# Kernel tuning notes

Measured on AMD Instinct MI355X. Metric: run time of the kernel, lower is better.

## Reference

```python
import jax, jax.numpy as jnp
import numpy as np
from jax import lax

B, N, IN_DIM = 8, 196, 2048
C = 256          # conv_channels / subspace dim
G = 1            # relation_glimpse


def _dilated_conv(x, w, b, dil):
    # x: [B,N,N,Cin], w: [3,3,Cin,Cout], SAME padding, rhs dilation per source
    y = lax.conv_general_dilated(x, w, window_strides=(1, 1), padding='SAME',
                                 rhs_dilation=dil,
                                 dimension_numbers=('NHWC', 'HWIO', 'NHWC'))
    return y + b


def _rel_map(X):
    # X: [B,N,N,G] -> symmetric add, move glimpse to axis 1, softmax over N*N
    Xs = X + jnp.transpose(X, (0, 2, 1, 3))          # [B,N,N,G]
    m = jnp.transpose(Xs, (0, 3, 2, 1))              # [B,G,N,N]
    bsz, g, n, _ = m.shape
    m = jax.nn.softmax(m.reshape(bsz, g, n * n), axis=2)
    return m.reshape(bsz, g, n, n)


def setup_inputs() -> dict:
    key = jax.random.key(0)
    ks = jax.random.split(key, 8)
    s = lambda *sh: 1.0 / np.sqrt(sh[-2] if len(sh) > 1 else sh[0])
    return {
        'x': jax.random.normal(ks[0], (B, N, IN_DIM), jnp.float32),
        'w_prj': jax.random.normal(ks[1], (IN_DIM, C), jnp.float32) * 0.02,
        'b_prj': jnp.zeros((C,), jnp.float32),
        'w01': jax.random.normal(ks[2], (C, C // 2), jnp.float32) * 0.06,
        'b01': jnp.zeros((C // 2,), jnp.float32),
        'w02': jax.random.normal(ks[3], (C // 2, C // 4), jnp.float32) * 0.09,
        'b02': jnp.zeros((C // 4,), jnp.float32),
        'w03': jax.random.normal(ks[4], (C // 4, G), jnp.float32) * 0.125,
        'b03': jnp.zeros((G,), jnp.float32),
        'w1': jax.random.normal(ks[5], (3, 3, C, C // 2), jnp.float32) * 0.02,
        'b1': jnp.zeros((C // 2,), jnp.float32),
        'w2': jax.random.normal(ks[6], (3, 3, C // 2, C // 4), jnp.float32) * 0.03,
        'b2': jnp.zeros((C // 4,), jnp.float32),
        'w3': jax.random.normal(ks[7], (3, 3, C // 4, G), jnp.float32) * 0.04,
        'b3': jnp.zeros((G,), jnp.float32),
    }


def reference(x, w_prj, b_prj, w01, b01, w02, b02, w03, b03,
              w1, b1, w2, b2, w3, b3):
    # project to subspace: [B,N,C]
    sub = jnp.einsum('bnd,dc->bnc', x, w_prj) + b_prj
    # pairwise outer product: pair[b,i,j,c] = sub[b,i,c]*sub[b,j,c]
    pair = sub[:, :, None, :] * sub[:, None, :, :]          # [B,N,N,C]

    # branch 0: stacked 1x1 convs (pointwise) with relu; dropout = identity (eval)
    X0 = jax.nn.relu(jnp.einsum('bijc,cd->bijd', pair, w01) + b01)
    X0 = jax.nn.relu(jnp.einsum('bijc,cd->bijd', X0, w02) + b02)
    X0 = jax.nn.relu(jnp.einsum('bijc,cd->bijd', X0, w03) + b03)  # [B,N,N,G]
    rel_map0 = _rel_map(X0)                                  # [B,G,N,N]

    # branch 1: stacked 3x3 dilated convs, dilations (1,1),(1,2),(1,4)
    X1 = jax.nn.relu(_dilated_conv(pair, w1, b1, (1, 1)))
    X1 = jax.nn.relu(_dilated_conv(X1, w2, b2, (1, 2)))
    X1 = jax.nn.relu(_dilated_conv(X1, w3, b3, (1, 4)))      # [B,N,N,G]
    rel_map1 = _rel_map(X1)

    # aggregation over glimpses: rel_x = sum_g (map1[g]@x + map0[g]@x) / (2G)
    rel_x = (jnp.einsum('bgij,bjd->bid', rel_map1, x) +
             jnp.einsum('bgij,bjd->bid', rel_map0, x)) / (2.0 * G)
    return rel_x.reshape(x.shape[0], -1)                     # [B, N*in_dim]
```

## Files before the change

kernel.cpp:

```cpp
#include <hip/hip_runtime.h>
#include <cmath>

#define N_TOK 196
#define NPX   38416
#define CDIM  256

typedef _Float16 f16;
typedef __attribute__((ext_vector_type(8))) _Float16 half8;
typedef __attribute__((ext_vector_type(4))) float f32x4;

__global__ __launch_bounds__(256) void proj_mfma(
    const float* __restrict__ A,
    const float* __restrict__ B,
    float* __restrict__ P)
{
    __shared__ f16 As[128 * 40];
    __shared__ f16 Bs[128 * 40];
    int tid = threadIdx.x;
    int n0 = blockIdx.x * 128, m0 = blockIdx.y * 128;
    int kz = blockIdx.z;
    int wave = tid >> 6, lane = tid & 63;
    int quad = lane >> 4, l16 = lane & 15;

    f32x4 zero = {0.f, 0.f, 0.f, 0.f};
    f32x4 acc[2][8];
    #pragma unroll
    for (int mt = 0; mt < 2; ++mt)
        #pragma unroll
        for (int nt = 0; nt < 8; ++nt) acc[mt][nt] = zero;

    for (int k0 = kz * 256; k0 < kz * 256 + 256; k0 += 32) {
        __syncthreads();
        #pragma unroll
        for (int s = 0; s < 4; ++s) {
            int idx = tid + s * 256;
            int m = idx >> 3, kq = idx & 7;
            int gm = m0 + m;
            float4 v = make_float4(0.f, 0.f, 0.f, 0.f);
            if (gm < 1568) v = *(const float4*)(A + (size_t)gm * 2048 + k0 + kq * 4);
            f16* d = As + m * 40 + kq * 4;
            d[0] = (f16)v.x; d[1] = (f16)v.y; d[2] = (f16)v.z; d[3] = (f16)v.w;
        }
        #pragma unroll
        for (int s = 0; s < 4; ++s) {
            int idx = tid + s * 256;
            int nq = idx & 31, kk = idx >> 5;
            float4 v = *(const float4*)(B + (size_t)(k0 + kk) * 256 + n0 + nq * 4);
            Bs[(nq * 4 + 0) * 40 + kk] = (f16)v.x;
            Bs[(nq * 4 + 1) * 40 + kk] = (f16)v.y;
            Bs[(nq * 4 + 2) * 40 + kk] = (f16)v.z;
            Bs[(nq * 4 + 3) * 40 + kk] = (f16)v.w;
        }
        __syncthreads();
        half8 a[2];
        #pragma unroll
        for (int mt = 0; mt < 2; ++mt)
            a[mt] = *(const half8*)(As + (wave * 32 + mt * 16 + l16) * 40 + quad * 8);
        #pragma unroll
        for (int nt = 0; nt < 8; ++nt) {
            half8 bf = *(const half8*)(Bs + (nt * 16 + l16) * 40 + quad * 8);
            acc[0][nt] = __builtin_amdgcn_mfma_f32_16x16x32_f16(a[0], bf, acc[0][nt], 0, 0, 0);
            acc[1][nt] = __builtin_amdgcn_mfma_f32_16x16x32_f16(a[1], bf, acc[1][nt], 0, 0, 0);
        }
    }
    float* Pz = P + (size_t)kz * 401408;
    #pragma unroll
    for (int mt = 0; mt < 2; ++mt) {
        #pragma unroll
        for (int nt = 0; nt < 8; ++nt) {
            int gn = n0 + nt * 16 + l16;
            #pragma unroll
            for (int r = 0; r < 4; ++r) {
                int gm = m0 + wave * 32 + mt * 16 + quad * 4 + r;
                if (gm < 1568) Pz[(size_t)gm * 256 + gn] = acc[mt][nt][r];
            }
        }
    }
}

__global__ void reduce_subh(const float* __restrict__ P,
                            const float* __restrict__ bias,
                            f16* __restrict__ subh)
{
    int e = blockIdx.x * 256 + threadIdx.x;
    if (e >= 401408) return;
    float s = bias[e & 255];
    #pragma unroll
    for (int z = 0; z < 8; ++z) s += P[(size_t)z * 401408 + e];
    subh[e] = (f16)s;
}

__global__ void cvt_wt(const float* __restrict__ w, f16* __restrict__ wt,
                       int Kc, int D, int total)
{
    int e = blockIdx.x * 256 + threadIdx.x;
    if (e >= total) return;
    int td = Kc * D;
    int tap = e / td, r = e - tap * td;
    int c = r / D, d = r - c * D;
    wt[(size_t)(tap * D + d) * Kc + c] = (f16)w[e];
}

__global__ void cvt_wfrag(const float* __restrict__ w, f16* __restrict__ wf,
                          int Kc, int D, int taps)
{
    int tiles = D >> 4, kch = Kc >> 5;
    int total = taps * tiles * kch * 64;
    int e = blockIdx.x * 256 + threadIdx.x;
    if (e >= total) return;
    int lane = e & 63;
    int rest = e >> 6;
    int k = rest % kch; rest /= kch;
    int tile = rest % tiles;
    int tap = rest / tiles;
    int l16 = lane & 15, quad = lane >> 4;
    const float* src = w + ((size_t)tap * Kc + k * 32 + quad * 8) * D + tile * 16 + l16;
    f16* dst = wf + (size_t)e * 8;
    #pragma unroll
    for (int j = 0; j < 8; ++j) dst[j] = (f16)src[(size_t)j * D];
}

__global__ __launch_bounds__(256) void cvt_xT(const float* __restrict__ x,
                                              f16* __restrict__ xht)
{
    __shared__ float t[32][33];
    int b = blockIdx.z;
    int i0 = blockIdx.y * 32, n0 = blockIdx.x * 32;
    const float* xb = x + (size_t)b * 196 * 2048;
    for (int e = threadIdx.x; e < 1024; e += 256) {
        int r = e >> 5, c = e & 31;
        int gi = i0 + r;
        t[r][c] = (gi < 196) ? xb[(size_t)gi * 2048 + n0 + c] : 0.f;
    }
    __syncthreads();
    f16* xb2 = xht + (size_t)b * 2048 * 200;
    for (int e = threadIdx.x; e < 1024; e += 256) {
        int nl = e >> 5, il = e & 31;
        int gi = i0 + il, gn = n0 + nl;
        if (gi < 200) xb2[(size_t)gn * 200 + gi] = (f16)t[il][nl];
    }
}

__global__ __launch_bounds__(256, 2) void conv1_mfma(
    const f16* __restrict__ sub_h,
    const f16* __restrict__ w1f,
    const float* __restrict__ b1,
    f16* __restrict__ Y1h)
{
    __shared__ f16 sh[17408];
    f16* SJ = sh;
    f16* SI = sh + 8976;
    f16* OT = sh;

    int b = blockIdx.z;
    int i0 = blockIdx.y * 8, j0 = blockIdx.x * 32;
    int tid = threadIdx.x;
    const f16* subB = sub_h + (size_t)b * N_TOK * CDIM;

    uint4 zz = make_uint4(0, 0, 0, 0);
    for (int e = tid; e < 1088; e += 256) {
        int r = e >> 5, q = e & 31;
        int gj = j0 - 1 + r;
        uint4 v = zz;
        if (gj >= 0 && gj < N_TOK) v = *(const uint4*)(subB + gj * CDIM + q * 8);
        *(uint4*)(SJ + r * 264 + q * 8) = v;
    }
    for (int e = tid; e < 320; e += 256) {
        int r = e >> 5, q = e & 31;
        int gi = i0 - 1 + r;
        uint4 v = zz;
        if (gi >= 0 && gi < N_TOK) v = *(const uint4*)(subB + gi * CDIM + q * 8);
        *(uint4*)(SI + r * 264 + q * 8) = v;
    }
    __syncthreads();

    int wave = tid >> 6, lane = tid & 63;
    int quad = lane >> 4, l16 = lane & 15;
    int p  = wave >> 1;
    int dh = wave & 1;
    int d0 = dh * 64;

    float bias_r[4];
    #pragma unroll
    for (int n = 0; n < 4; ++n) bias_r[n] = b1[d0 + n * 16 + l16];

    const f16* wbase = w1f + (size_t)lane * 8 + (size_t)dh * 4 * 4096;

    int lb = blockIdx.x + 7 * (blockIdx.y + 25 * blockIdx.z);
    int rot = (lb * 3 + wave) & 7;

    f32x4 zero = {0.f, 0.f, 0.f, 0.f};
    f32x4 acc[8][4];
    #pragma unroll
    for (int m = 0; m < 8; ++m)
        #pragma unroll
        for (int n = 0; n < 4; ++n) acc[m][n] = zero;

    for (int kk = 0; kk < 8; ++kk) {
        int k = (kk + rot) & 7;
        int c0 = k * 32;
        half8 si[6];
        #pragma unroll
        for (int r = 0; r < 6; ++r)
            si[r] = *(const half8*)(SI + (p * 4 + r) * 264 + c0 + quad * 8);
        half8 sj[2][3];
        #pragma unroll
        for (int jf = 0; jf < 2; ++jf)
            #pragma unroll
            for (int dd = 0; dd < 3; ++dd)
                sj[jf][dd] = *(const half8*)(SJ + (jf * 16 + l16 + dd) * 264 + c0 + quad * 8);

        #pragma unroll
        for (int dj = 0; dj < 3; ++dj) {
            half8 bf[3][4];
            #pragma unroll
            for (int di = 0; di < 3; ++di)
                #pragma unroll
                for (int n = 0; n < 4; ++n)
                    bf[di][n] = *(const half8*)(wbase + (size_t)(di * 3 + dj) * 32768
                                                + n * 4096 + k * 512);
            #pragma unroll
            for (int r = 0; r < 6; ++r) {
                half8 a0 = si[r] * sj[0][dj];
                half8 a1 = si[r] * sj[1][dj];
                #pragma unroll
                for (int di = 0; di < 3; ++di) {
                    int i = r - di;
                    if (i < 0 || i > 3) continue;
                    #pragma unroll
                    for (int n = 0; n < 4; ++n) {
                        acc[i * 2 + 0][n] = __builtin_amdgcn_mfma_f32_16x16x32_f16(
                            a0, bf[di][n], acc[i * 2 + 0][n], 0, 0, 0);
                        acc[i * 2 + 1][n] = __builtin_amdgcn_mfma_f32_16x16x32_f16(
                            a1, bf[di][n], acc[i * 2 + 1][n], 0, 0, 0);
                    }
                }
            }
        }
    }

    __syncthreads();
    f16* Yb = Y1h + (size_t)b * NPX * 128;
    #pragma unroll
    for (int ph = 0; ph < 2; ++ph) {
        if (p == ph) {
            #pragma unroll
            for (int i = 0; i < 4; ++i)
                #pragma unroll
                for (int jf = 0; jf < 2; ++jf) {
                    int m = i * 2 + jf;
                    #pragma unroll
                    for (int n = 0; n < 4; ++n) {
                        int dl = d0 + n * 16 + l16;
                        #pragma unroll
                        for (int r = 0; r < 4; ++r) {
                            int pxl = i * 32 + jf * 16 + quad * 4 + r;
                            OT[pxl * 136 + dl] = (f16)fmaxf(acc[m][n][r] + bias_r[n], 0.f);
                        }
                    }
                }
        }
        __syncthreads();
        for (int e = tid; e < 2048; e += 256) {
            int pxl = e >> 4, q = e & 15;
            int gi = i0 + ph * 4 + (pxl >> 5), gj = j0 + (pxl & 31);
            if (gi < N_TOK && gj < N_TOK)
                *(uint4*)(Yb + ((size_t)gi * N_TOK + gj) * 128 + q * 8) =
                    *(const uint4*)(OT + pxl * 136 + q * 8);
        }
        __syncthreads();
    }
}

__global__ __launch_bounds__(256, 2) void conv2_mfma(
    const f16* __restrict__ Y1h, const f16* __restrict__ w2f,
    const float* __restrict__ b2, f16* __restrict__ Y2h)
{
    __shared__ f16 sh[29376];
    f16* Ys = sh;
    f16* OT = sh;

    int b = blockIdx.z;
    int i0 = blockIdx.y * 4, j0 = blockIdx.x * 32;
    int tid = threadIdx.x;
    const f16* Yb = Y1h + (size_t)b * NPX * 128;

    uint4 zz = make_uint4(0, 0, 0, 0);
    for (int e = tid; e < 3456; e += 256) {
        int ir = e / 576, rem = e - ir * 576;
        int jq = rem >> 4, q = rem & 15;
        int gi = i0 - 1 + ir, gj = j0 - 2 + jq;
        uint4 v = zz;
        if (gi >= 0 && gi < N_TOK && gj >= 0 && gj < N_TOK)
            v = *(const uint4*)(Yb + ((size_t)gi * N_TOK + gj) * 128 + q * 8);
        *(uint4*)(Ys + (ir * 36 + jq) * 136 + q * 8) = v;
    }
    __syncthreads();

    int wave = tid >> 6, lane = tid & 63;
    int quad = lane >> 4, l16 = lane & 15;
    int ii = wave;

    const f16* wbase = w2f + (size_t)lane * 8;

    f32x4 zero = {0.f, 0.f, 0.f, 0.f};
    f32x4 acc[2][4];
    #pragma unroll
    for (int jf = 0; jf < 2; ++jf)
        #pragma unroll
        for (int n = 0; n < 4; ++n) acc[jf][n] = zero;

    #pragma unroll
    for (int tap = 0; tap < 9; ++tap) {
        int di = tap / 3 - 1, dj2 = (tap % 3 - 1) * 2;
        #pragma unroll
        for (int k = 0; k < 4; ++k) {
            int c0 = k * 32;
            half8 a0 = *(const half8*)(Ys + ((ii + di + 1) * 36 + l16 + dj2 + 2) * 136
                                       + c0 + quad * 8);
            half8 a1 = *(const half8*)(Ys + ((ii + di + 1) * 36 + 16 + l16 + dj2 + 2) * 136
                                       + c0 + quad * 8);
            #pragma unroll
            for (int n = 0; n < 4; ++n) {
                half8 bf = *(const half8*)(wbase + (size_t)tap * 8192 + n * 2048 + k * 512);
                acc[0][n] = __builtin_amdgcn_mfma_f32_16x16x32_f16(a0, bf, acc[0][n], 0, 0, 0);
                acc[1][n] = __builtin_amdgcn_mfma_f32_16x16x32_f16(a1, bf, acc[1][n], 0, 0, 0);
            }
        }
    }
    __syncthreads();
    #pragma unroll
    for (int jf = 0; jf < 2; ++jf)
        #pragma unroll
        for (int n = 0; n < 4; ++n) {
            int d = n * 16 + l16;
            float bias = b2[d];
            #pragma unroll
            for (int r = 0; r < 4; ++r) {
                int px = ii * 32 + jf * 16 + quad * 4 + r;
                OT[px * 72 + d] = (f16)fmaxf(acc[jf][n][r] + bias, 0.f);
            }
        }
    __syncthreads();
    f16* Zb = Y2h + (size_t)b * NPX * 64;
    for (int e = tid; e < 1024; e += 256) {
        int px = e >> 3, q = e & 7;
        int i = i0 + (px >> 5), j = j0 + (px & 31);
        if (j < N_TOK)
            *(uint4*)(Zb + ((size_t)i * N_TOK + j) * 64 + q * 8) =
                *(const uint4*)(OT + px * 72 + q * 8);
    }
}

__global__ __launch_bounds__(256) void conv3_s(
    const f16* __restrict__ Y2h, const float* __restrict__ w3,
    const float* __restrict__ b3, float* __restrict__ X1)
{
    __shared__ f16 Ys[10 * 40 * 68];
    __shared__ float ws[576];
    int b = blockIdx.z;
    int i0 = blockIdx.y * 8, j0 = blockIdx.x * 32;
    int tid = threadIdx.x;
    const f16* Yb = Y2h + (size_t)b * NPX * 64;
    for (int e = tid; e < 576; e += 256) ws[e] = w3[e];
    uint4 zz = make_uint4(0, 0, 0, 0);
    for (int e = tid; e < 3200; e += 256) {
        int r = e / 320, rem = e - r * 320;
        int jq = rem >> 3, q = rem & 7;
        int gi = i0 - 1 + r, gj = j0 - 4 + jq;
        uint4 v = zz;
        if (gi >= 0 && gi < N_TOK && gj >= 0 && gj < N_TOK)
            v = *(const uint4*)(Yb + ((size_t)gi * N_TOK + gj) * 64 + q * 8);
        *(uint4*)(Ys + (r * 40 + jq) * 68 + q * 8) = v;
    }
    __syncthreads();
    int q = tid & 7, jl = (tid >> 3) & 31;
    float* Xb = X1 + (size_t)b * NPX;
    float bb = b3[0];
    #pragma unroll
    for (int il = 0; il < 8; ++il) {
        float s = 0.f;
        #pragma unroll
        for (int tap = 0; tap < 9; ++tap) {
            int di = tap / 3 - 1, dj4 = (tap % 3 - 1) * 4;
            half8 h = *(const half8*)(Ys + ((il + 1 + di) * 40 + jl + 4 + dj4) * 68 + q * 8);
            #pragma unroll
            for (int e = 0; e < 8; ++e) s += (float)h[e] * ws[tap * 64 + q * 8 + e];
        }
        s += __shfl_xor(s, 1);
        s += __shfl_xor(s, 2);
        s += __shfl_xor(s, 4);
        if (q == 0) {
            int gi = i0 + il, gj = j0 + jl;
            if (gi < N_TOK && gj < N_TOK)
                Xb[gi * N_TOK + gj] = fmaxf(s + bb, 0.f);
        }
    }
}

__global__ __launch_bounds__(256, 2) void branch0_mfma(
    const f16* __restrict__ sub_h,
    const f16* __restrict__ w01t,
    const float* __restrict__ b01,
    const f16* __restrict__ w02t,
    const float* __restrict__ b02,
    const float* __restrict__ w03, const float* __restrict__ b03,
    float* __restrict__ X0)
{
    __shared__ f16 sh[32000];
    __shared__ float W3s[64];
    f16* SJ = sh;
    f16* SI = sh + 8448;
    f16* BW = sh + 9472;
    f16* H1 = sh + 14592;
    f16* H2 = sh;

    int b = blockIdx.z;
    int i0 = blockIdx.y * 4, j0 = blockIdx.x * 32;
    int tid = threadIdx.x;
    const f16* subB = sub_h + (size_t)b * N_TOK * CDIM;

    uint4 zz = make_uint4(0, 0, 0, 0);
    for (int e = tid; e < 1024; e += 256) {
        int r = e >> 5, q = e & 31;
        int gj = j0 + r;
        uint4 v = zz;
        if (gj < N_TOK) v = *(const uint4*)(subB + gj * CDIM + q * 8);
        *(uint4*)(SJ + r * 264 + q * 8) = v;
    }
    if (tid < 128) {
        int r = tid >> 5, q = tid & 31;
        int gi = i0 + r;
        uint4 v = zz;
        if (gi < N_TOK) v = *(const uint4*)(subB + gi * CDIM + q * 8);
        *(uint4*)(SI + r * 256 + q * 8) = v;
    }
    if (tid < 64) W3s[tid] = w03[tid];

    int wave = tid >> 6, lane = tid & 63;
    int quad = lane >> 4, l16 = lane & 15;
    int ii = wave;

    f32x4 zero = {0.f, 0.f, 0.f, 0.f};
    f32x4 acc[2][8];
    #pragma unroll
    for (int t = 0; t < 2; ++t)
        #pragma unroll
        for (int n = 0; n < 8; ++n) acc[t][n] = zero;

    for (int c0 = 0; c0 < 256; c0 += 32) {
        __syncthreads();
        for (int e = tid; e < 512; e += 256) {
            int d = e >> 2, q = e & 3;
            *(uint4*)(BW + d * 40 + q * 8) =
                *(const uint4*)(w01t + (size_t)d * 256 + c0 + q * 8);
        }
        __syncthreads();
        half8 sib = *(const half8*)(SI + ii * 256 + c0 + quad * 8);
        half8 a0 = sib * *(const half8*)(SJ + l16 * 264 + c0 + quad * 8);
        half8 a1 = sib * *(const half8*)(SJ + (l16 + 16) * 264 + c0 + quad * 8);
        #pragma unroll
        for (int n = 0; n < 8; ++n) {
            half8 bf = *(const half8*)(BW + (n * 16 + l16) * 40 + quad * 8);
            acc[0][n] = __builtin_amdgcn_mfma_f32_16x16x32_f16(a0, bf, acc[0][n], 0, 0, 0);
            acc[1][n] = __builtin_amdgcn_mfma_f32_16x16x32_f16(a1, bf, acc[1][n], 0, 0, 0);
        }
    }
    #pragma unroll
    for (int t = 0; t < 2; ++t)
        #pragma unroll
        for (int n = 0; n < 8; ++n) {
            int d = n * 16 + l16;
            float bias = b01[d];
            #pragma unroll
            for (int r = 0; r < 4; ++r) {
                int px = ii * 32 + t * 16 + quad * 4 + r;
                H1[px * 136 + d] = (f16)fmaxf(acc[t][n][r] + bias, 0.f);
            }
        }

    f32x4 acc2[2][4];
    #pragma unroll
    for (int t = 0; t < 2; ++t)
        #pragma unroll
        for (int n = 0; n < 4; ++n) acc2[t][n] = zero;

    for (int c0 = 0; c0 < 128; c0 += 32) {
        __syncthreads();
        {
            int d = tid >> 2, q = tid & 3;
            if (d < 64)
                *(uint4*)(BW + d * 40 + q * 8) =
                    *(const uint4*)(w02t + (size_t)d * 128 + c0 + q * 8);
        }
        __syncthreads();
        half8 a0 = *(const half8*)(H1 + (ii * 32 + l16) * 136 + c0 + quad * 8);
        half8 a1 = *(const half8*)(H1 + (ii * 32 + 16 + l16) * 136 + c0 + quad * 8);
        #pragma unroll
        for (int n = 0; n < 4; ++n) {
            half8 bf = *(const half8*)(BW + (n * 16 + l16) * 40 + quad * 8);
            acc2[0][n] = __builtin_amdgcn_mfma_f32_16x16x32_f16(a0, bf, acc2[0][n], 0, 0, 0);
            acc2[1][n] = __builtin_amdgcn_mfma_f32_16x16x32_f16(a1, bf, acc2[1][n], 0, 0, 0);
        }
    }
    #pragma unroll
    for (int t = 0; t < 2; ++t)
        #pragma unroll
        for (int n = 0; n < 4; ++n) {
            int e = n * 16 + l16;
            float bias = b02[e];
            #pragma unroll
            for (int r = 0; r < 4; ++r) {
                int px = ii * 32 + t * 16 + quad * 4 + r;
                H2[px * 72 + e] = (f16)fmaxf(acc2[t][n][r] + bias, 0.f);
            }
        }
    __syncthreads();
    if (tid < 128) {
        int px = tid;
        float s = b03[0];
        const f16* h = H2 + px * 72;
        #pragma unroll 8
        for (int c = 0; c < 64; ++c) s += (float)h[c] * W3s[c];
        int i = i0 + (px >> 5), j = j0 + (px & 31);
        if (j < N_TOK)
            X0[(size_t)b * NPX + i * N_TOK + j] = fmaxf(s, 0.f);
    }
}

__global__ __launch_bounds__(1024) void symsoftmax(float* __restrict__ X0,
                                                   float* __restrict__ X1)
{
    __shared__ float red[32];
    __shared__ float red2[32];
    float* X = (blockIdx.y ? X1 : X0) + (long long)blockIdx.x * NPX;
    int tid = threadIdx.x;
    float v[38];
    float mx = -3.0e38f;
    #pragma unroll
    for (int p = 0; p < 38; ++p) {
        int e = tid + p * 1024;
        if (e < NPX) {
            int i = e / 196, j = e - i * 196;
            float t = X[e] + X[j * 196 + i];
            v[p] = t;
            mx = fmaxf(mx, t);
        } else v[p] = -3.0e38f;
    }
    #pragma unroll
    for (int off = 32; off > 0; off >>= 1) mx = fmaxf(mx, __shfl_xor(mx, off));
    if ((tid & 63) == 0) red[tid >> 6] = mx;
    __syncthreads();
    if (tid < 64) {
        float m = (tid < 16) ? red[tid] : -3.0e38f;
        #pragma unroll
        for (int off = 8; off > 0; off >>= 1) m = fmaxf(m, __shfl_xor(m, off));
        if (tid == 0) red[0] = m;
    }
    __syncthreads();
    mx = red[0];
    float s = 0.f;
    #pragma unroll
    for (int p = 0; p < 38; ++p) {
        int e = tid + p * 1024;
        float ex = (e < NPX) ? expf(v[p] - mx) : 0.f;
        v[p] = ex;
        s += ex;
    }
    #pragma unroll
    for (int off = 32; off > 0; off >>= 1) s += __shfl_xor(s, off);
    if ((tid & 63) == 0) red2[tid >> 6] = s;
    __syncthreads();
    if (tid < 64) {
        float m = (tid < 16) ? red2[tid] : 0.f;
        #pragma unroll
        for (int off = 8; off > 0; off >>= 1) m += __shfl_xor(m, off);
        if (tid == 0) red2[0] = m;
    }
    __syncthreads();
    float scale = 0.5f / red2[0];
    #pragma unroll
    for (int p = 0; p < 38; ++p) {
        int e = tid + p * 1024;
        if (e < NPX) X[e] = v[p] * scale;
    }
}

__global__ void combine_ph(const float* __restrict__ X0,
                           const float* __restrict__ X1,
                           f16* __restrict__ Ph)
{
    int e = blockIdx.x * 256 + threadIdx.x;
    if (e >= 8 * 196 * 200) return;
    int j = e % 200;
    int row = e / 200;
    f16 v = (f16)0.f;
    if (j < 196) {
        int src = row * 196 + j;
        v = (f16)((X0[src] + X1[src]) * 512.0f);
    }
    Ph[e] = v;
}

__global__ __launch_bounds__(256, 2) void gemm_out(
    const f16* __restrict__ Ph, const f16* __restrict__ xht,
    float* __restrict__ out)
{
    __shared__ f16 As[64 * 72];
    __shared__ f16 Bs[128 * 72];
    int b = blockIdx.z;
    int n0 = blockIdx.x * 128, m0 = blockIdx.y * 64;
    int tid = threadIdx.x;
    const f16* Pb = Ph + (size_t)b * 196 * 200;
    const f16* xb = xht + (size_t)b * 2048 * 200;

    int wave = tid >> 6, lane = tid & 63;
    int quad = lane >> 4, l16 = lane & 15;

    f32x4 zero = {0.f, 0.f, 0.f, 0.f};
    f32x4 acc[8];
    #pragma unroll
    for (int n = 0; n < 8; ++n) acc[n] = zero;

    uint4 zz = make_uint4(0, 0, 0, 0);
    for (int k0 = 0; k0 < 256; k0 += 64) {
        __syncthreads();
        for (int e = tid; e < 512; e += 256) {
            int r = e >> 3, q = e & 7;
            int gm = m0 + r, k = k0 + q * 8;
            uint4 v = zz;
            if (gm < 196 && k < 200) v = *(const uint4*)(Pb + (size_t)gm * 200 + k);
            *(uint4*)(As + r * 72 + q * 8) = v;
        }
        for (int e = tid; e < 1024; e += 256) {
            int r = e >> 3, q = e & 7;
            int k = k0 + q * 8;
            uint4 v = zz;
            if (k < 200) v = *(const uint4*)(xb + (size_t)(n0 + r) * 200 + k);
            *(uint4*)(Bs + r * 72 + q * 8) = v;
        }
        __syncthreads();
        #pragma unroll
        for (int ks = 0; ks < 2; ++ks) {
            half8 a = *(const half8*)(As + (wave * 16 + l16) * 72 + ks * 32 + quad * 8);
            #pragma unroll
            for (int n = 0; n < 8; ++n) {
                half8 bf = *(const half8*)(Bs + (n * 16 + l16) * 72 + ks * 32 + quad * 8);
                acc[n] = __builtin_amdgcn_mfma_f32_16x16x32_f16(a, bf, acc[n], 0, 0, 0);
            }
        }
    }
    int m_base = m0 + wave * 16 + quad * 4;
    float* ob = out + (size_t)b * 196 * 2048;
    #pragma unroll
    for (int n = 0; n < 8; ++n) {
        int gn = n0 + n * 16 + l16;
        #pragma unroll
        for (int r = 0; r < 4; ++r) {
            int gm = m_base + r;
            if (gm < 196) ob[(size_t)gm * 2048 + gn] = acc[n][r] * (1.0f / 512.0f);
        }
    }
}

extern "C" void kernel_launch(void* const* d_in, const int* in_sizes, int n_in,
                              void* d_out, int out_size, void* d_ws, size_t ws_size,
                              hipStream_t stream)
{
    (void)in_sizes; (void)n_in; (void)out_size; (void)ws_size;
    const float* x     = (const float*)d_in[0];
    const float* w_prj = (const float*)d_in[1];
    const float* b_prj = (const float*)d_in[2];
    const float* w01   = (const float*)d_in[3];
    const float* b01   = (const float*)d_in[4];
    const float* w02   = (const float*)d_in[5];
    const float* b02   = (const float*)d_in[6];
    const float* w03   = (const float*)d_in[7];
    const float* b03   = (const float*)d_in[8];
    const float* w1    = (const float*)d_in[9];
    const float* b1    = (const float*)d_in[10];
    const float* w2    = (const float*)d_in[11];
    const float* b2    = (const float*)d_in[12];
    const float* w3    = (const float*)d_in[13];
    const float* b3    = (const float*)d_in[14];

    char* W = (char*)d_ws;
    float* part = (float*)(W + 0);
    float* X0   = (float*)(W + 12845056);
    float* X1   = (float*)(W + 14074368);
    f16*   subh = (f16*)(W + 15303680);
    f16*   w1f  = (f16*)(W + 16106496);
    f16*   w2f  = (f16*)(W + 16696320);
    f16*   w01t = (f16*)(W + 16843776);
    f16*   w02t = (f16*)(W + 16909312);
    f16*   Ph   = (f16*)(W + 16925696);
    f16*   xht  = (f16*)(W + 17552896);
    f16*   Y1h  = (f16*)(W + 24106496);
    f16*   Y2h  = (f16*)(W + 102782464);

    proj_mfma<<<dim3(2, 13, 8), 256, 0, stream>>>(x, w_prj, part);
    reduce_subh<<<dim3(1568), 256, 0, stream>>>(part, b_prj, subh);

    cvt_wfrag<<<dim3(144), 256, 0, stream>>>(w1, w1f, 256, 128, 9);
    cvt_wfrag<<<dim3(36),  256, 0, stream>>>(w2, w2f, 128, 64, 9);
    cvt_wt<<<dim3(128),  256, 0, stream>>>(w01, w01t, 256, 128, 32768);
    cvt_wt<<<dim3(32),   256, 0, stream>>>(w02, w02t, 128, 64, 8192);
    cvt_xT<<<dim3(64, 7, 8), 256, 0, stream>>>(x, xht);

    branch0_mfma<<<dim3(7, 49, 8), 256, 0, stream>>>(
        subh, w01t, b01, w02t, b02, w03, b03, X0);

    conv1_mfma<<<dim3(7, 25, 8), 256, 0, stream>>>(subh, w1f, b1, Y1h);
    conv2_mfma<<<dim3(7, 49, 8), 256, 0, stream>>>(Y1h, w2f, b2, Y2h);
    conv3_s<<<dim3(7, 25, 8), 256, 0, stream>>>(Y2h, w3, b3, X1);

    symsoftmax<<<dim3(8, 2), 1024, 0, stream>>>(X0, X1);

    combine_ph<<<dim3(1225), 256, 0, stream>>>(X0, X1, Ph);

    gemm_out<<<dim3(16, 4, 8), 256, 0, stream>>>(Ph, xht, (float*)d_out);
}
```

Before: 513.9 us.

## Split conv1 work across 16 waves per block with smaller per-wave tiles

Conv1 now launches 1024 threads per block instead of 256. Each of the 16 waves computes 2 output rows by 32 output channels instead of 4 rows by 64 channels, which cuts accumulator registers from 32 to 8 fragments per wave. The goal is higher occupancy and more latency hiding, without changing the tile or the shared-memory footprint. The cost is that each wave reloads the si/sj operands and the weight fragments relative to the work it does, so redundant LDS and global weight loads go up.

```diff
diff --git a/kernel.cpp b/kernel.cpp
--- a/kernel.cpp
+++ b/kernel.cpp
@@ -141,7 +141,7 @@
     }
 }
 
-__global__ __launch_bounds__(256, 2) void conv1_mfma(
+__global__ __launch_bounds__(1024, 4) void conv1_mfma(
     const f16* __restrict__ sub_h,
     const f16* __restrict__ w1f,
     const float* __restrict__ b1,
@@ -158,14 +158,14 @@
     const f16* subB = sub_h + (size_t)b * N_TOK * CDIM;
 
     uint4 zz = make_uint4(0, 0, 0, 0);
-    for (int e = tid; e < 1088; e += 256) {
+    for (int e = tid; e < 1088; e += 1024) {
         int r = e >> 5, q = e & 31;
         int gj = j0 - 1 + r;
         uint4 v = zz;
         if (gj >= 0 && gj < N_TOK) v = *(const uint4*)(subB + gj * CDIM + q * 8);
         *(uint4*)(SJ + r * 264 + q * 8) = v;
     }
-    for (int e = tid; e < 320; e += 256) {
+    for (int e = tid; e < 320; e += 1024) {
         int r = e >> 5, q = e & 31;
         int gi = i0 - 1 + r;
         uint4 v = zz;
@@ -176,63 +176,59 @@
 
     int wave = tid >> 6, lane = tid & 63;
     int quad = lane >> 4, l16 = lane & 15;
-    int p  = wave >> 1;
-    int dh = wave & 1;
-    int d0 = dh * 64;
-
-    float bias_r[4];
-    #pragma unroll
-    for (int n = 0; n < 4; ++n) bias_r[n] = b1[d0 + n * 16 + l16];
-
-    const f16* wbase = w1f + (size_t)lane * 8 + (size_t)dh * 4 * 4096;
+    int ig = wave >> 2;
+    int dg = wave & 3;
+    int d0 = dg * 32;
+
+    float bias_r[2];
+    #pragma unroll
+    for (int n = 0; n < 2; ++n) bias_r[n] = b1[d0 + n * 16 + l16];
+
+    const f16* wbase = w1f + (size_t)lane * 8 + (size_t)dg * 2 * 4096;
 
     int lb = blockIdx.x + 7 * (blockIdx.y + 25 * blockIdx.z);
-    int rot = (lb * 3 + wave) & 7;
+    int rot = (lb * 5 + wave) & 7;
 
     f32x4 zero = {0.f, 0.f, 0.f, 0.f};
-    f32x4 acc[8][4];
-    #pragma unroll
-    for (int m = 0; m < 8; ++m)
-        #pragma unroll
-        for (int n = 0; n < 4; ++n) acc[m][n] = zero;
+    f32x4 acc[4][2];
+    #pragma unroll
+    for (int a = 0; a < 4; ++a)
+        #pragma unroll
+        for (int n = 0; n < 2; ++n) acc[a][n] = zero;
 
     for (int kk = 0; kk < 8; ++kk) {
         int k = (kk + rot) & 7;
         int c0 = k * 32;
-        half8 si[6];
-        #pragma unroll
-        for (int r = 0; r < 6; ++r)
-            si[r] = *(const half8*)(SI + (p * 4 + r) * 264 + c0 + quad * 8);
-        half8 sj[2][3];
-        #pragma unroll
-        for (int jf = 0; jf < 2; ++jf)
-            #pragma unroll
-            for (int dd = 0; dd < 3; ++dd)
-                sj[jf][dd] = *(const half8*)(SJ + (jf * 16 + l16 + dd) * 264 + c0 + quad * 8);
+        half8 si[4];
+        #pragma unroll
+        for (int r = 0; r < 4; ++r)
+            si[r] = *(const half8*)(SI + (ig * 2 + r) * 264 + c0 + quad * 8);
 
         #pragma unroll
         for (int dj = 0; dj < 3; ++dj) {
-            half8 bf[3][4];
+            half8 sj0 = *(const half8*)(SJ + (l16 + dj) * 264 + c0 + quad * 8);
+            half8 sj1 = *(const half8*)(SJ + (16 + l16 + dj) * 264 + c0 + quad * 8);
+            half8 bf[3][2];
             #pragma unroll
             for (int di = 0; di < 3; ++di)
                 #pragma unroll
-                for (int n = 0; n < 4; ++n)
+                for (int n = 0; n < 2; ++n)
                     bf[di][n] = *(const half8*)(wbase + (size_t)(di * 3 + dj) * 32768
                                                 + n * 4096 + k * 512);
             #pragma unroll
-            for (int r = 0; r < 6; ++r) {
-                half8 a0 = si[r] * sj[0][dj];
-                half8 a1 = si[r] * sj[1][dj];
+            for (int r = 0; r < 4; ++r) {
+                half8 a0 = si[r] * sj0;
+                half8 a1 = si[r] * sj1;
                 #pragma unroll
                 for (int di = 0; di < 3; ++di) {
-                    int i = r - di;
-                    if (i < 0 || i > 3) continue;
+                    int m = r - di;
+                    if (m < 0 || m > 1) continue;
                     #pragma unroll
-                    for (int n = 0; n < 4; ++n) {
-                        acc[i * 2 + 0][n] = __builtin_amdgcn_mfma_f32_16x16x32_f16(
-                            a0, bf[di][n], acc[i * 2 + 0][n], 0, 0, 0);
-                        acc[i * 2 + 1][n] = __builtin_amdgcn_mfma_f32_16x16x32_f16(
-                            a1, bf[di][n], acc[i * 2 + 1][n], 0, 0, 0);
+                    for (int n = 0; n < 2; ++n) {
+                        acc[m * 2 + 0][n] = __builtin_amdgcn_mfma_f32_16x16x32_f16(
+                            a0, bf[di][n], acc[m * 2 + 0][n], 0, 0, 0);
+                        acc[m * 2 + 1][n] = __builtin_amdgcn_mfma_f32_16x16x32_f16(
+                            a1, bf[di][n], acc[m * 2 + 1][n], 0, 0, 0);
                     }
                 }
             }
@@ -243,25 +239,26 @@
     f16* Yb = Y1h + (size_t)b * NPX * 128;
     #pragma unroll
     for (int ph = 0; ph < 2; ++ph) {
-        if (p == ph) {
-            #pragma unroll
-            for (int i = 0; i < 4; ++i)
+        if ((ig >> 1) == ph) {
+            #pragma unroll
+            for (int m = 0; m < 2; ++m)
                 #pragma unroll
                 for (int jf = 0; jf < 2; ++jf) {
-                    int m = i * 2 + jf;
+                    int al = m * 2 + jf;
+                    int il = ig * 2 + m - ph * 4;
                     #pragma unroll
-                    for (int n = 0; n < 4; ++n) {
+                    for (int n = 0; n < 2; ++n) {
                         int dl = d0 + n * 16 + l16;
                         #pragma unroll
                         for (int r = 0; r < 4; ++r) {
-                            int pxl = i * 32 + jf * 16 + quad * 4 + r;
-                            OT[pxl * 136 + dl] = (f16)fmaxf(acc[m][n][r] + bias_r[n], 0.f);
+                            int pxl = il * 32 + jf * 16 + quad * 4 + r;
+                            OT[pxl * 136 + dl] = (f16)fmaxf(acc[al][n][r] + bias_r[n], 0.f);
                         }
                     }
                 }
         }
         __syncthreads();
-        for (int e = tid; e < 2048; e += 256) {
+        for (int e = tid; e < 2048; e += 1024) {
             int pxl = e >> 4, q = e & 15;
             int gi = i0 + ph * 4 + (pxl >> 5), gj = j0 + (pxl & 31);
             if (gi < N_TOK && gj < N_TOK)
@@ -710,7 +707,7 @@
     branch0_mfma<<<dim3(7, 49, 8), 256, 0, stream>>>(
         subh, w01t, b01, w02t, b02, w03, b03, X0);
 
-    conv1_mfma<<<dim3(7, 25, 8), 256, 0, stream>>>(subh, w1f, b1, Y1h);
+    conv1_mfma<<<dim3(7, 25, 8), 1024, 0, stream>>>(subh, w1f, b1, Y1h);
     conv2_mfma<<<dim3(7, 49, 8), 256, 0, stream>>>(Y1h, w2f, b2, Y2h);
     conv3_s<<<dim3(7, 25, 8), 256, 0, stream>>>(Y2h, w3, b3, X1);
 
```

New measurement: 559.2 us. 8.8% more time.
